# Kernel optimization log

Measured on AMD Instinct MI355X. Metric: run time of the kernel, lower is better.

## Reference

```python
import jax, jax.numpy as jnp
import numpy as np

N_NODES = 100000
N_EDGES = 600000
D = 128


def setup_inputs() -> dict:
    key = jax.random.key(0)
    k1, k2, k3, k4, k5, k6 = jax.random.split(key, 6)
    feat = jax.random.normal(k1, (N_NODES, D), dtype=jnp.float32)
    src = jax.random.randint(k2, (N_EDGES,), 0, N_NODES, dtype=jnp.int64)
    dst = jax.random.randint(k3, (N_EDGES,), 0, N_NODES, dtype=jnp.int64)
    W_neigh = jax.random.normal(k4, (D, D), dtype=jnp.float32) * (1.0 / np.sqrt(D))
    b_neigh = jax.random.normal(k5, (D,), dtype=jnp.float32) * 0.02
    W_self = jax.random.normal(k6, (D, D), dtype=jnp.float32) * (1.0 / np.sqrt(D))
    return {"feat": feat, "src": src, "dst": dst,
            "W_neigh": W_neigh, "b_neigh": b_neigh, "W_self": W_self}


def reference(feat, src, dst, W_neigh, b_neigh, W_self):
    # DGL GraphConv(norm='none'): sum-aggregate neighbor features, then linear.
    # agg[i] = sum_{(s->i) in E} feat[s]
    agg = jax.ops.segment_sum(feat[src], dst, num_segments=feat.shape[0])  # [N, D]
    neigh_feat = agg @ W_neigh + b_neigh                                   # [N, Dout]
    self_feat = feat @ W_self                                              # [N, Dout]
    return neigh_feat + self_feat
```

## Files before the change

### kernel.cpp

```cpp
#include <hip/hip_runtime.h>

#define DF 128
#define CAP 16
#define GR 64
#define PBLK 256

typedef __attribute__((ext_vector_type(8))) short short8;
typedef __attribute__((ext_vector_type(4))) float v4f;

__device__ __forceinline__ unsigned short f2bf(float x) {
    unsigned u = __float_as_uint(x);
    unsigned r = (u + 0x7FFFu + ((u >> 16) & 1u)) >> 16;
    return (unsigned short)r;
}
__device__ __forceinline__ float bf2f(unsigned short h) {
    return __uint_as_float((unsigned)h << 16);
}
__device__ __forceinline__ unsigned pack2(float a, float b) {
    return (unsigned)f2bf(a) | ((unsigned)f2bf(b) << 16);
}

__global__ __launch_bounds__(256) void prep_kernel(
    const int* __restrict__ idx32, int nE, int* __restrict__ hdr,
    const float* __restrict__ Wn, const float* __restrict__ Ws,
    unsigned short* __restrict__ Bt, int* __restrict__ counts, int cnt_ints,
    unsigned short* __restrict__ Ybf, int M)
{
    const int b = blockIdx.x;
    const int t = threadIdx.x;
    if (b == 0) {
        __shared__ int sh;
        if (t == 0) sh = 0;
        __syncthreads();
        int found = 0;
        for (int i = t; i < 2048 && i < nE; i += 256)
            if (idx32[2 * i + 1] != 0) found = 1;
        if (found) sh = 1;
        __syncthreads();
        if (t == 0) { hdr[0] = sh; hdr[1] = 0; }
        if (t < 64)
            reinterpret_cast<unsigned*>(Ybf + (size_t)M * DF)[t] = 0u;
    } else if (b <= 128) {
        int idx = (b - 1) * 256 + t;
        int n = idx >> 7, k = idx & 127;
        float v = (n < DF) ? Wn[(size_t)k * DF + n] : Ws[(size_t)k * DF + (n - DF)];
        Bt[idx] = f2bf(v);
    } else {
        int off = ((b - 129) * 256 + t) * 4;
        if (off < cnt_ints)
            *reinterpret_cast<int4*>(counts + off) = make_int4(0, 0, 0, 0);
    }
}

__global__ __launch_bounds__(256) void fused_kernel(
    const float* __restrict__ feat, const unsigned short* __restrict__ Bt,
    const float* __restrict__ bias, unsigned short* __restrict__ Ybf,
    float* __restrict__ out, int M,
    const void* __restrict__ src, const void* __restrict__ dst, int nE,
    int* __restrict__ hdr, int* __restrict__ counts, int* __restrict__ buckets,
    int2* __restrict__ ovf)
{
    const int t = threadIdx.x;

    if (blockIdx.x < PBLK) {
        const int is32 = hdr[0];
        const int stride = PBLK * 256;
        if (is32) {
            const int* sp = (const int*)src;
            const int* dp = (const int*)dst;
            for (int e = blockIdx.x * 256 + t; e < nE; e += stride) {
                int s = sp[e], d = dp[e];
                int pos = atomicAdd(&counts[d], 1);
                if (pos < CAP) {
                    buckets[(size_t)d * CAP + pos] = s;
                } else {
                    int oi = atomicAdd(&hdr[1], 1);
                    ovf[oi] = make_int2(s, d);
                }
            }
        } else {
            const long long* sp = (const long long*)src;
            const long long* dp = (const long long*)dst;
            for (int e = blockIdx.x * 256 + t; e < nE; e += stride) {
                int s = (int)sp[e], d = (int)dp[e];
                int pos = atomicAdd(&counts[d], 1);
                if (pos < CAP) {
                    buckets[(size_t)d * CAP + pos] = s;
                } else {
                    int oi = atomicAdd(&hdr[1], 1);
                    ovf[oi] = make_int2(s, d);
                }
            }
        }
        return;
    }

    __shared__ unsigned short As[GR][136];
    __shared__ unsigned short Ys[GR][136];

    const int wave = t >> 6;
    const int lane = t & 63;
    const int nl   = lane & 15;
    const int quad = lane >> 4;
    const int block_row = (blockIdx.x - PBLK) * GR;

    {
        const float* base = feat + (size_t)block_row * DF;
#pragma unroll
        for (int it = 0; it < 8; it++) {
            const int idx = t * 4 + it * 1024;
            const int row = idx >> 7, col = idx & 127;
            float4 v;
            if (block_row + row < M)
                v = *reinterpret_cast<const float4*>(base + idx);
            else
                v = make_float4(0.f, 0.f, 0.f, 0.f);
            uint2 pk;
            pk.x = pack2(v.x, v.y);
            pk.y = pack2(v.z, v.w);
            *reinterpret_cast<uint2*>(&As[row][col]) = pk;
        }
    }

    const int n0 = wave * 64;
    short8 bfrag[4][4];
#pragma unroll
    for (int ct = 0; ct < 4; ct++)
#pragma unroll
        for (int kk = 0; kk < 4; kk++)
            bfrag[ct][kk] = *reinterpret_cast<const short8*>(
                Bt + (size_t)(n0 + ct * 16 + nl) * DF + kk * 32 + quad * 8);

    float bcol[4];
#pragma unroll
    for (int ct = 0; ct < 4; ct++) {
        int n = n0 + ct * 16 + nl;
        bcol[ct] = (n >= DF) ? bias[n - DF] : 0.f;
    }

    __syncthreads();

#pragma unroll
    for (int rt = 0; rt < 4; rt++) {
        short8 afrag[4];
#pragma unroll
        for (int kk = 0; kk < 4; kk++)
            afrag[kk] = *reinterpret_cast<const short8*>(
                &As[rt * 16 + nl][kk * 32 + quad * 8]);
#pragma unroll
        for (int ct = 0; ct < 4; ct++) {
            v4f acc = {0.f, 0.f, 0.f, 0.f};
#pragma unroll
            for (int kk = 0; kk < 4; kk++)
                acc = __builtin_amdgcn_mfma_f32_16x16x32_bf16(
                    afrag[kk], bfrag[ct][kk], acc, 0, 0, 0);
            const int n = n0 + ct * 16 + nl;
            const int lrow = rt * 16 + quad * 4;
            if (n < DF) {
#pragma unroll
                for (int r = 0; r < 4; r++)
                    Ys[lrow + r][n] = f2bf(acc[r]);
            } else {
#pragma unroll
                for (int r = 0; r < 4; r++) {
                    const int grow = block_row + lrow + r;
                    if (grow < M)
                        out[(size_t)grow * DF + (n - DF)] = acc[r] + bcol[ct];
                }
            }
        }
    }

    __syncthreads();

    {
        const int row = t >> 2;
        const int cb  = (t & 3) * 32;
        const int grow = block_row + row;
        if (grow < M) {
            const uint4* srcp = reinterpret_cast<const uint4*>(&Ys[row][cb]);
            uint4* dstp = reinterpret_cast<uint4*>(Ybf + (size_t)grow * DF + cb);
            dstp[0] = srcp[0];
            dstp[1] = srcp[1];
            dstp[2] = srcp[2];
            dstp[3] = srcp[3];
        }
    }
}

__global__ __launch_bounds__(256) void gather_kernel(
    const unsigned short* __restrict__ Ybf,
    const int* __restrict__ counts, const int* __restrict__ buckets,
    const int* __restrict__ hdr, const int2* __restrict__ ovf,
    float* __restrict__ out, int M, int ngroups)
{
    const int gid  = blockIdx.x * 256 + threadIdx.x;
    const int grp  = gid >> 4;
    const int lane = gid & 15;
    const size_t lo = (size_t)lane * 8;

#define LDY(s) (*reinterpret_cast<const uint4*>(Ybf + (size_t)(s) * DF + lo))
#define ACC8(Y) do { \
        a0 += bf2f((unsigned short)((Y).x)); a1 += bf2f((unsigned short)((Y).x >> 16)); \
        a2 += bf2f((unsigned short)((Y).y)); a3 += bf2f((unsigned short)((Y).y >> 16)); \
        a4 += bf2f((unsigned short)((Y).z)); a5 += bf2f((unsigned short)((Y).z >> 16)); \
        a6 += bf2f((unsigned short)((Y).w)); a7 += bf2f((unsigned short)((Y).w >> 16)); \
    } while (0)

    if (grp < M) {
        const int node = grp;
        const int deg_raw = counts[node];
        const int deg = min(deg_raw, CAP);
        const int* b = buckets + (size_t)node * CAP;
        float* op = out + (size_t)node * DF + lo;

        float a0 = 0.f, a1 = 0.f, a2 = 0.f, a3 = 0.f;
        float a4 = 0.f, a5 = 0.f, a6 = 0.f, a7 = 0.f;

        int4 sa = *reinterpret_cast<const int4*>(b);
        int4 sb = *reinterpret_cast<const int4*>(b + 4);
        const int i0 = (0 < deg) ? sa.x : M;
        const int i1 = (1 < deg) ? sa.y : M;
        const int i2 = (2 < deg) ? sa.z : M;
        const int i3 = (3 < deg) ? sa.w : M;
        const int i4 = (4 < deg) ? sb.x : M;
        const int i5 = (5 < deg) ? sb.y : M;
        const int i6 = (6 < deg) ? sb.z : M;
        const int i7 = (7 < deg) ? sb.w : M;

        uint4 y0 = LDY(i0);
        uint4 y1 = LDY(i1);
        uint4 y2 = LDY(i2);
        uint4 y3 = LDY(i3);
        uint4 y4 = LDY(i4);
        uint4 y5 = LDY(i5);
        uint4 y6 = LDY(i6);
        uint4 y7 = LDY(i7);
        float4 o0 = *reinterpret_cast<const float4*>(op);
        float4 o1 = *reinterpret_cast<const float4*>(op + 4);
        __builtin_amdgcn_sched_barrier(0);
        ACC8(y0); ACC8(y1); ACC8(y2); ACC8(y3);
        ACC8(y4); ACC8(y5); ACC8(y6); ACC8(y7);

        if (deg > 8) {
            int4 sc = *reinterpret_cast<const int4*>(b + 8);
            int4 sd = *reinterpret_cast<const int4*>(b + 12);
            const int j0 = ( 8 < deg) ? sc.x : M;
            const int j1 = ( 9 < deg) ? sc.y : M;
            const int j2 = (10 < deg) ? sc.z : M;
            const int j3 = (11 < deg) ? sc.w : M;
            const int j4 = (12 < deg) ? sd.x : M;
            const int j5 = (13 < deg) ? sd.y : M;
            const int j6 = (14 < deg) ? sd.z : M;
            const int j7 = (15 < deg) ? sd.w : M;
            uint4 z0 = LDY(j0);
            uint4 z1 = LDY(j1);
            uint4 z2 = LDY(j2);
            uint4 z3 = LDY(j3);
            uint4 z4 = LDY(j4);
            uint4 z5 = LDY(j5);
            uint4 z6 = LDY(j6);
            uint4 z7 = LDY(j7);
            __builtin_amdgcn_sched_barrier(0);
            ACC8(z0); ACC8(z1); ACC8(z2); ACC8(z3);
            ACC8(z4); ACC8(z5); ACC8(z6); ACC8(z7);
        }

        if (deg_raw <= CAP) {
            o0.x += a0; o0.y += a1; o0.z += a2; o0.w += a3;
            o1.x += a4; o1.y += a5; o1.z += a6; o1.w += a7;
            *reinterpret_cast<float4*>(op)     = o0;
            *reinterpret_cast<float4*>(op + 4) = o1;
        } else {
            unsafeAtomicAdd(op + 0, a0);
            unsafeAtomicAdd(op + 1, a1);
            unsafeAtomicAdd(op + 2, a2);
            unsafeAtomicAdd(op + 3, a3);
            unsafeAtomicAdd(op + 4, a4);
            unsafeAtomicAdd(op + 5, a5);
            unsafeAtomicAdd(op + 6, a6);
            unsafeAtomicAdd(op + 7, a7);
        }
    }

    int n_ovf = hdr[1];
    for (int i = grp; i < n_ovf; i += ngroups) {
        int2 sd = ovf[i];
        uint4 y = LDY(sd.x);
        float* p = out + (size_t)sd.y * DF + lo;
        unsafeAtomicAdd(p + 0, bf2f((unsigned short)(y.x)));
        unsafeAtomicAdd(p + 1, bf2f((unsigned short)(y.x >> 16)));
        unsafeAtomicAdd(p + 2, bf2f((unsigned short)(y.y)));
        unsafeAtomicAdd(p + 3, bf2f((unsigned short)(y.y >> 16)));
        unsafeAtomicAdd(p + 4, bf2f((unsigned short)(y.z)));
        unsafeAtomicAdd(p + 5, bf2f((unsigned short)(y.z >> 16)));
        unsafeAtomicAdd(p + 6, bf2f((unsigned short)(y.w)));
        unsafeAtomicAdd(p + 7, bf2f((unsigned short)(y.w >> 16)));
    }
#undef LDY
#undef ACC8
}

extern "C" void kernel_launch(void* const* d_in, const int* in_sizes, int n_in,
                              void* d_out, int out_size, void* d_ws, size_t ws_size,
                              hipStream_t stream) {
    const float* feat = (const float*)d_in[0];
    const void*  src  = d_in[1];
    const void*  dst  = d_in[2];
    const float* Wn   = (const float*)d_in[3];
    const float* bias = (const float*)d_in[4];
    const float* Wsf  = (const float*)d_in[5];
    float* out = (float*)d_out;

    const int M  = in_sizes[0] / DF;
    const int nE = in_sizes[1];

    const size_t cnt_off   = 256;
    const size_t cnt_bytes = (((size_t)(M + 1) * 4) + 255) & ~(size_t)255;
    const size_t bkt_off   = cnt_off + cnt_bytes;
    const size_t bkt_bytes = (size_t)M * CAP * sizeof(int);
    const size_t bt_off    = (bkt_off + bkt_bytes + 255) & ~(size_t)255;
    const size_t bt_bytes  = (size_t)256 * DF * sizeof(unsigned short);
    const size_t y_off     = bt_off + bt_bytes;
    const size_t y_bytes   = (size_t)(M + 1) * DF * sizeof(unsigned short);
    const size_t ovf_off   = (y_off + y_bytes + 255) & ~(size_t)255;

    int*            hdr     = (int*)d_ws;
    int*            counts  = (int*)((char*)d_ws + cnt_off);
    int*            buckets = (int*)((char*)d_ws + bkt_off);
    unsigned short* Bt      = (unsigned short*)((char*)d_ws + bt_off);
    unsigned short* Ybf     = (unsigned short*)((char*)d_ws + y_off);
    int2*           ovf     = (int2*)((char*)d_ws + ovf_off);

    const int cnt_ints = (int)(cnt_bytes / 4);
    const int nzb = (cnt_ints + 1023) / 1024;
    prep_kernel<<<1 + 128 + nzb, 256, 0, stream>>>(
        (const int*)src, nE, hdr, Wn, Wsf, Bt, counts, cnt_ints, Ybf, M);

    const int gemm_blocks = (M + GR - 1) / GR;
    fused_kernel<<<PBLK + gemm_blocks, 256, 0, stream>>>(
        feat, Bt, bias, Ybf, out, M, src, dst, nE,
        hdr, counts, buckets, ovf);

    const int gablocks = (int)(((long long)M * 16 + 255) / 256);
    const int ngroups = gablocks * 16;
    gather_kernel<<<gablocks, 256, 0, stream>>>(
        Ybf, counts, buckets, hdr, ovf, out, M, ngroups);
}
```

Baseline: 193.9 us.

## Aggregate bf16 features before GEMM and fuse gather with combined K=256 matmul

Reorders the computation from transform-then-aggregate to aggregate-then-transform. Features are converted to bf16 in the prep kernel, and edge placement becomes its own kernel. A single kernel then gathers neighbour rows, builds a [agg | self] tile in shared memory, and runs one K=256 MFMA GEMM that writes the output once. This removes the Ybf intermediate write and read, plus the read-modify-write of out in the gather. The cost is a longer GEMM K dimension, an extra bf16 rounding of the aggregated sum, and a serial scan of the overflow list for high-degree nodes.

```diff
diff --git a/kernel.cpp b/kernel.cpp
--- a/kernel.cpp
+++ b/kernel.cpp
@@ -1,9 +1,10 @@
 #include <hip/hip_runtime.h>
 
 #define DF 128
+#define KX 256
 #define CAP 16
 #define GR 64
-#define PBLK 256
+#define PBLK 1024
 
 typedef __attribute__((ext_vector_type(8))) short short8;
 typedef __attribute__((ext_vector_type(4))) float v4f;
@@ -23,8 +24,9 @@
 __global__ __launch_bounds__(256) void prep_kernel(
     const int* __restrict__ idx32, int nE, int* __restrict__ hdr,
     const float* __restrict__ Wn, const float* __restrict__ Ws,
-    unsigned short* __restrict__ Bt, int* __restrict__ counts, int cnt_ints,
-    unsigned short* __restrict__ Ybf, int M)
+    unsigned short* __restrict__ Bt2, int* __restrict__ counts, int cnt_ints,
+    const float* __restrict__ feat, unsigned short* __restrict__ Fbf,
+    int M, int nzb)
 {
     const int b = blockIdx.x;
     const int t = threadIdx.x;
@@ -39,167 +41,106 @@
         __syncthreads();
         if (t == 0) { hdr[0] = sh; hdr[1] = 0; }
         if (t < 64)
-            reinterpret_cast<unsigned*>(Ybf + (size_t)M * DF)[t] = 0u;
+            reinterpret_cast<unsigned*>(Fbf + (size_t)M * DF)[t] = 0u;
     } else if (b <= 128) {
         int idx = (b - 1) * 256 + t;
-        int n = idx >> 7, k = idx & 127;
-        float v = (n < DF) ? Wn[(size_t)k * DF + n] : Ws[(size_t)k * DF + (n - DF)];
-        Bt[idx] = f2bf(v);
-    } else {
+        int n = idx >> 8, k = idx & 255;
+        float v = (k < DF) ? Wn[(size_t)k * DF + n]
+                           : Ws[(size_t)(k - DF) * DF + n];
+        Bt2[idx] = f2bf(v);
+    } else if (b <= 128 + nzb) {
         int off = ((b - 129) * 256 + t) * 4;
         if (off < cnt_ints)
             *reinterpret_cast<int4*>(counts + off) = make_int4(0, 0, 0, 0);
+    } else {
+        const long long base = ((long long)(b - 129 - nzb) * 2048 + t * 8);
+        const long long total = (long long)M * DF;
+        if (base + 8 <= total) {
+            float4 v0 = *reinterpret_cast<const float4*>(feat + base);
+            float4 v1 = *reinterpret_cast<const float4*>(feat + base + 4);
+            uint4 pk;
+            pk.x = pack2(v0.x, v0.y);
+            pk.y = pack2(v0.z, v0.w);
+            pk.z = pack2(v1.x, v1.y);
+            pk.w = pack2(v1.z, v1.w);
+            *reinterpret_cast<uint4*>(Fbf + base) = pk;
+        }
     }
 }
 
-__global__ __launch_bounds__(256) void fused_kernel(
-    const float* __restrict__ feat, const unsigned short* __restrict__ Bt,
-    const float* __restrict__ bias, unsigned short* __restrict__ Ybf,
-    float* __restrict__ out, int M,
+__global__ __launch_bounds__(256) void place_kernel(
     const void* __restrict__ src, const void* __restrict__ dst, int nE,
     int* __restrict__ hdr, int* __restrict__ counts, int* __restrict__ buckets,
     int2* __restrict__ ovf)
 {
     const int t = threadIdx.x;
-
-    if (blockIdx.x < PBLK) {
-        const int is32 = hdr[0];
-        const int stride = PBLK * 256;
-        if (is32) {
-            const int* sp = (const int*)src;
-            const int* dp = (const int*)dst;
-            for (int e = blockIdx.x * 256 + t; e < nE; e += stride) {
-                int s = sp[e], d = dp[e];
-                int pos = atomicAdd(&counts[d], 1);
-                if (pos < CAP) {
-                    buckets[(size_t)d * CAP + pos] = s;
-                } else {
-                    int oi = atomicAdd(&hdr[1], 1);
-                    ovf[oi] = make_int2(s, d);
-                }
-            }
-        } else {
-            const long long* sp = (const long long*)src;
-            const long long* dp = (const long long*)dst;
-            for (int e = blockIdx.x * 256 + t; e < nE; e += stride) {
-                int s = (int)sp[e], d = (int)dp[e];
-                int pos = atomicAdd(&counts[d], 1);
-                if (pos < CAP) {
-                    buckets[(size_t)d * CAP + pos] = s;
-                } else {
-                    int oi = atomicAdd(&hdr[1], 1);
-                    ovf[oi] = make_int2(s, d);
-                }
-            }
-        }
-        return;
+    const int is32 = hdr[0];
+    const int stride = PBLK * 256;
+    if (is32) {
+        const int* sp = (const int*)src;
+        const int* dp = (const int*)dst;
+        for (int e = blockIdx.x * 256 + t; e < nE; e += stride) {
+            int s = sp[e], d = dp[e];
+            int pos = atomicAdd(&counts[d], 1);
+            if (pos < CAP) {
+                buckets[(size_t)d * CAP + pos] = s;
+            } else {
+                int oi = atomicAdd(&hdr[1], 1);
+                ovf[oi] = make_int2(s, d);
+            }
+        }
+    } else {
+        const long long* sp = (const long long*)src;
+        const long long* dp = (const long long*)dst;
+        for (int e = blockIdx.x * 256 + t; e < nE; e += stride) {
+            int s = (int)sp[e], d = (int)dp[e];
+            int pos = atomicAdd(&counts[d], 1);
+            if (pos < CAP) {
+                buckets[(size_t)d * CAP + pos] = s;
+            } else {
+                int oi = atomicAdd(&hdr[1], 1);
+                ovf[oi] = make_int2(s, d);
+            }
+        }
     }
-
-    __shared__ unsigned short As[GR][136];
-    __shared__ unsigned short Ys[GR][136];
+}
+
+__global__ __launch_bounds__(256) void agg_gemm_kernel(
+    const unsigned short* __restrict__ Fbf, const unsigned short* __restrict__ Bt2,
+    const float* __restrict__ bias, float* __restrict__ out, int M,
+    const int* __restrict__ counts, const int* __restrict__ buckets,
+    const int* __restrict__ hdr, const int2* __restrict__ ovf)
+{
+    __shared__ unsigned short As[GR][KX + 8];
+
+    const int t = threadIdx.x;
+    const int block_row = blockIdx.x * GR;
 
     const int wave = t >> 6;
     const int lane = t & 63;
     const int nl   = lane & 15;
     const int quad = lane >> 4;
-    const int block_row = (blockIdx.x - PBLK) * GR;
+
+    const int n0 = wave * 32;
+    short8 bfrag[2][8];
+#pragma unroll
+    for (int ct = 0; ct < 2; ct++)
+#pragma unroll
+        for (int kk = 0; kk < 8; kk++)
+            bfrag[ct][kk] = *reinterpret_cast<const short8*>(
+                Bt2 + (size_t)(n0 + ct * 16 + nl) * KX + kk * 32 + quad * 8);
+    float bcol[2];
+#pragma unroll
+    for (int ct = 0; ct < 2; ct++)
+        bcol[ct] = bias[n0 + ct * 16 + nl];
 
     {
-        const float* base = feat + (size_t)block_row * DF;
-#pragma unroll
-        for (int it = 0; it < 8; it++) {
-            const int idx = t * 4 + it * 1024;
-            const int row = idx >> 7, col = idx & 127;
-            float4 v;
-            if (block_row + row < M)
-                v = *reinterpret_cast<const float4*>(base + idx);
-            else
-                v = make_float4(0.f, 0.f, 0.f, 0.f);
-            uint2 pk;
-            pk.x = pack2(v.x, v.y);
-            pk.y = pack2(v.z, v.w);
-            *reinterpret_cast<uint2*>(&As[row][col]) = pk;
-        }
-    }
-
-    const int n0 = wave * 64;
-    short8 bfrag[4][4];
-#pragma unroll
-    for (int ct = 0; ct < 4; ct++)
-#pragma unroll
-        for (int kk = 0; kk < 4; kk++)
-            bfrag[ct][kk] = *reinterpret_cast<const short8*>(
-                Bt + (size_t)(n0 + ct * 16 + nl) * DF + kk * 32 + quad * 8);
-
-    float bcol[4];
-#pragma unroll
-    for (int ct = 0; ct < 4; ct++) {
-        int n = n0 + ct * 16 + nl;
-        bcol[ct] = (n >= DF) ? bias[n - DF] : 0.f;
-    }
-
-    __syncthreads();
-
-#pragma unroll
-    for (int rt = 0; rt < 4; rt++) {
-        short8 afrag[4];
-#pragma unroll
-        for (int kk = 0; kk < 4; kk++)
-            afrag[kk] = *reinterpret_cast<const short8*>(
-                &As[rt * 16 + nl][kk * 32 + quad * 8]);
-#pragma unroll
-        for (int ct = 0; ct < 4; ct++) {
-            v4f acc = {0.f, 0.f, 0.f, 0.f};
-#pragma unroll
-            for (int kk = 0; kk < 4; kk++)
-                acc = __builtin_amdgcn_mfma_f32_16x16x32_bf16(
-                    afrag[kk], bfrag[ct][kk], acc, 0, 0, 0);
-            const int n = n0 + ct * 16 + nl;
-            const int lrow = rt * 16 + quad * 4;
-            if (n < DF) {
-#pragma unroll
-                for (int r = 0; r < 4; r++)
-                    Ys[lrow + r][n] = f2bf(acc[r]);
-            } else {
-#pragma unroll
-                for (int r = 0; r < 4; r++) {
-                    const int grow = block_row + lrow + r;
-                    if (grow < M)
-                        out[(size_t)grow * DF + (n - DF)] = acc[r] + bcol[ct];
-                }
-            }
-        }
-    }
-
-    __syncthreads();
-
-    {
-        const int row = t >> 2;
-        const int cb  = (t & 3) * 32;
-        const int grow = block_row + row;
-        if (grow < M) {
-            const uint4* srcp = reinterpret_cast<const uint4*>(&Ys[row][cb]);
-            uint4* dstp = reinterpret_cast<uint4*>(Ybf + (size_t)grow * DF + cb);
-            dstp[0] = srcp[0];
-            dstp[1] = srcp[1];
-            dstp[2] = srcp[2];
-            dstp[3] = srcp[3];
-        }
-    }
-}
-
-__global__ __launch_bounds__(256) void gather_kernel(
-    const unsigned short* __restrict__ Ybf,
-    const int* __restrict__ counts, const int* __restrict__ buckets,
-    const int* __restrict__ hdr, const int2* __restrict__ ovf,
-    float* __restrict__ out, int M, int ngroups)
-{
-    const int gid  = blockIdx.x * 256 + threadIdx.x;
-    const int grp  = gid >> 4;
-    const int lane = gid & 15;
-    const size_t lo = (size_t)lane * 8;
-
-#define LDY(s) (*reinterpret_cast<const uint4*>(Ybf + (size_t)(s) * DF + lo))
+        const int gi = t >> 4;
+        const int li = t & 15;
+        const size_t lo = (size_t)li * 8;
+        const int n_ovf = hdr[1];
+
+#define LDF(s) (*reinterpret_cast<const uint4*>(Fbf + (size_t)(s) * DF + lo))
 #define ACC8(Y) do { \
         a0 += bf2f((unsigned short)((Y).x)); a1 += bf2f((unsigned short)((Y).x >> 16)); \
         a2 += bf2f((unsigned short)((Y).y)); a3 += bf2f((unsigned short)((Y).y >> 16)); \
@@ -207,98 +148,110 @@
         a6 += bf2f((unsigned short)((Y).w)); a7 += bf2f((unsigned short)((Y).w >> 16)); \
     } while (0)
 
-    if (grp < M) {
-        const int node = grp;
-        const int deg_raw = counts[node];
-        const int deg = min(deg_raw, CAP);
-        const int* b = buckets + (size_t)node * CAP;
-        float* op = out + (size_t)node * DF + lo;
-
-        float a0 = 0.f, a1 = 0.f, a2 = 0.f, a3 = 0.f;
-        float a4 = 0.f, a5 = 0.f, a6 = 0.f, a7 = 0.f;
-
-        int4 sa = *reinterpret_cast<const int4*>(b);
-        int4 sb = *reinterpret_cast<const int4*>(b + 4);
-        const int i0 = (0 < deg) ? sa.x : M;
-        const int i1 = (1 < deg) ? sa.y : M;
-        const int i2 = (2 < deg) ? sa.z : M;
-        const int i3 = (3 < deg) ? sa.w : M;
-        const int i4 = (4 < deg) ? sb.x : M;
-        const int i5 = (5 < deg) ? sb.y : M;
-        const int i6 = (6 < deg) ? sb.z : M;
-        const int i7 = (7 < deg) ? sb.w : M;
-
-        uint4 y0 = LDY(i0);
-        uint4 y1 = LDY(i1);
-        uint4 y2 = LDY(i2);
-        uint4 y3 = LDY(i3);
-        uint4 y4 = LDY(i4);
-        uint4 y5 = LDY(i5);
-        uint4 y6 = LDY(i6);
-        uint4 y7 = LDY(i7);
-        float4 o0 = *reinterpret_cast<const float4*>(op);
-        float4 o1 = *reinterpret_cast<const float4*>(op + 4);
-        __builtin_amdgcn_sched_barrier(0);
-        ACC8(y0); ACC8(y1); ACC8(y2); ACC8(y3);
-        ACC8(y4); ACC8(y5); ACC8(y6); ACC8(y7);
-
-        if (deg > 8) {
-            int4 sc = *reinterpret_cast<const int4*>(b + 8);
-            int4 sd = *reinterpret_cast<const int4*>(b + 12);
-            const int j0 = ( 8 < deg) ? sc.x : M;
-            const int j1 = ( 9 < deg) ? sc.y : M;
-            const int j2 = (10 < deg) ? sc.z : M;
-            const int j3 = (11 < deg) ? sc.w : M;
-            const int j4 = (12 < deg) ? sd.x : M;
-            const int j5 = (13 < deg) ? sd.y : M;
-            const int j6 = (14 < deg) ? sd.z : M;
-            const int j7 = (15 < deg) ? sd.w : M;
-            uint4 z0 = LDY(j0);
-            uint4 z1 = LDY(j1);
-            uint4 z2 = LDY(j2);
-            uint4 z3 = LDY(j3);
-            uint4 z4 = LDY(j4);
-            uint4 z5 = LDY(j5);
-            uint4 z6 = LDY(j6);
-            uint4 z7 = LDY(j7);
-            __builtin_amdgcn_sched_barrier(0);
-            ACC8(z0); ACC8(z1); ACC8(z2); ACC8(z3);
-            ACC8(z4); ACC8(z5); ACC8(z6); ACC8(z7);
-        }
-
-        if (deg_raw <= CAP) {
-            o0.x += a0; o0.y += a1; o0.z += a2; o0.w += a3;
-            o1.x += a4; o1.y += a5; o1.z += a6; o1.w += a7;
-            *reinterpret_cast<float4*>(op)     = o0;
-            *reinterpret_cast<float4*>(op + 4) = o1;
-        } else {
-            unsafeAtomicAdd(op + 0, a0);
-            unsafeAtomicAdd(op + 1, a1);
-            unsafeAtomicAdd(op + 2, a2);
-            unsafeAtomicAdd(op + 3, a3);
-            unsafeAtomicAdd(op + 4, a4);
-            unsafeAtomicAdd(op + 5, a5);
-            unsafeAtomicAdd(op + 6, a6);
-            unsafeAtomicAdd(op + 7, a7);
-        }
+#pragma unroll
+        for (int j = 0; j < 4; j++) {
+            const int r_local = gi * 4 + j;
+            const int grow = block_row + r_local;
+            const int deg_raw = (grow < M) ? counts[grow] : 0;
+            const int deg = min(deg_raw, CAP);
+            const int* b = buckets + (size_t)((grow < M) ? grow : 0) * CAP;
+
+            float a0 = 0.f, a1 = 0.f, a2 = 0.f, a3 = 0.f;
+            float a4 = 0.f, a5 = 0.f, a6 = 0.f, a7 = 0.f;
+
+            int4 sa = *reinterpret_cast<const int4*>(b);
+            int4 sb = *reinterpret_cast<const int4*>(b + 4);
+            const int i0 = (0 < deg) ? sa.x : M;
+            const int i1 = (1 < deg) ? sa.y : M;
+            const int i2 = (2 < deg) ? sa.z : M;
+            const int i3 = (3 < deg) ? sa.w : M;
+            const int i4 = (4 < deg) ? sb.x : M;
+            const int i5 = (5 < deg) ? sb.y : M;
+            const int i6 = (6 < deg) ? sb.z : M;
+            const int i7 = (7 < deg) ? sb.w : M;
+            uint4 y0 = LDF(i0);
+            uint4 y1 = LDF(i1);
+            uint4 y2 = LDF(i2);
+            uint4 y3 = LDF(i3);
+            uint4 y4 = LDF(i4);
+            uint4 y5 = LDF(i5);
+            uint4 y6 = LDF(i6);
+            uint4 y7 = LDF(i7);
+            uint4 sf = LDF((grow < M) ? grow : M);
+            ACC8(y0); ACC8(y1); ACC8(y2); ACC8(y3);
+            ACC8(y4); ACC8(y5); ACC8(y6); ACC8(y7);
+
+            if (deg > 8) {
+                int4 sc = *reinterpret_cast<const int4*>(b + 8);
+                int4 sd = *reinterpret_cast<const int4*>(b + 12);
+                const int j0 = ( 8 < deg) ? sc.x : M;
+                const int j1 = ( 9 < deg) ? sc.y : M;
+                const int j2 = (10 < deg) ? sc.z : M;
+                const int j3 = (11 < deg) ? sc.w : M;
+                const int j4 = (12 < deg) ? sd.x : M;
+                const int j5 = (13 < deg) ? sd.y : M;
+                const int j6 = (14 < deg) ? sd.z : M;
+                const int j7 = (15 < deg) ? sd.w : M;
+                uint4 z0 = LDF(j0);
+                uint4 z1 = LDF(j1);
+                uint4 z2 = LDF(j2);
+                uint4 z3 = LDF(j3);
+                uint4 z4 = LDF(j4);
+                uint4 z5 = LDF(j5);
+                uint4 z6 = LDF(j6);
+                uint4 z7 = LDF(j7);
+                ACC8(z0); ACC8(z1); ACC8(z2); ACC8(z3);
+                ACC8(z4); ACC8(z5); ACC8(z6); ACC8(z7);
+            }
+
+            if (deg_raw > CAP) {
+                for (int i = 0; i < n_ovf; i++) {
+                    int2 sd2 = ovf[i];
+                    if (sd2.y == grow) {
+                        uint4 y = LDF(sd2.x);
+                        ACC8(y);
+                    }
+                }
+            }
+
+            uint4 pk;
+            pk.x = pack2(a0, a1);
+            pk.y = pack2(a2, a3);
+            pk.z = pack2(a4, a5);
+            pk.w = pack2(a6, a7);
+            *reinterpret_cast<uint4*>(&As[r_local][lo])      = pk;
+            *reinterpret_cast<uint4*>(&As[r_local][DF + lo]) = sf;
+        }
+#undef LDF
+#undef ACC8
     }
 
-    int n_ovf = hdr[1];
-    for (int i = grp; i < n_ovf; i += ngroups) {
-        int2 sd = ovf[i];
-        uint4 y = LDY(sd.x);
-        float* p = out + (size_t)sd.y * DF + lo;
-        unsafeAtomicAdd(p + 0, bf2f((unsigned short)(y.x)));
-        unsafeAtomicAdd(p + 1, bf2f((unsigned short)(y.x >> 16)));
-        unsafeAtomicAdd(p + 2, bf2f((unsigned short)(y.y)));
-        unsafeAtomicAdd(p + 3, bf2f((unsigned short)(y.y >> 16)));
-        unsafeAtomicAdd(p + 4, bf2f((unsigned short)(y.z)));
-        unsafeAtomicAdd(p + 5, bf2f((unsigned short)(y.z >> 16)));
-        unsafeAtomicAdd(p + 6, bf2f((unsigned short)(y.w)));
-        unsafeAtomicAdd(p + 7, bf2f((unsigned short)(y.w >> 16)));
+    __syncthreads();
+
+#pragma unroll
+    for (int rt = 0; rt < 4; rt++) {
+        short8 afrag[8];
+#pragma unroll
+        for (int kk = 0; kk < 8; kk++)
+            afrag[kk] = *reinterpret_cast<const short8*>(
+                &As[rt * 16 + nl][kk * 32 + quad * 8]);
+#pragma unroll
+        for (int ct = 0; ct < 2; ct++) {
+            v4f acc = {0.f, 0.f, 0.f, 0.f};
+#pragma unroll
+            for (int kk = 0; kk < 8; kk++)
+                acc = __builtin_amdgcn_mfma_f32_16x16x32_bf16(
+                    afrag[kk], bfrag[ct][kk], acc, 0, 0, 0);
+            const int n = n0 + ct * 16 + nl;
+            const int lrow = rt * 16 + quad * 4;
+#pragma unroll
+            for (int r = 0; r < 4; r++) {
+                const int grow = block_row + lrow + r;
+                if (grow < M)
+                    out[(size_t)grow * DF + n] = acc[r] + bcol[ct];
+            }
+        }
     }
-#undef LDY
-#undef ACC8
 }
 
 extern "C" void kernel_launch(void* const* d_in, const int* in_sizes, int n_in,
@@ -316,34 +269,35 @@
     const int nE = in_sizes[1];
 
     const size_t cnt_off   = 256;
-    const size_t cnt_bytes = (((size_t)(M + 1) * 4) + 255) & ~(size_t)255;
+    const size_t cnt_bytes = (((size_t)(M + 64) * 4) + 255) & ~(size_t)255;
     const size_t bkt_off   = cnt_off + cnt_bytes;
     const size_t bkt_bytes = (size_t)M * CAP * sizeof(int);
     const size_t bt_off    = (bkt_off + bkt_bytes + 255) & ~(size_t)255;
-    const size_t bt_bytes  = (size_t)256 * DF * sizeof(unsigned short);
-    const size_t y_off     = bt_off + bt_bytes;
-    const size_t y_bytes   = (size_t)(M + 1) * DF * sizeof(unsigned short);
-    const size_t ovf_off   = (y_off + y_bytes + 255) & ~(size_t)255;
+    const size_t bt_bytes  = (size_t)DF * KX * sizeof(unsigned short);
+    const size_t f_off     = bt_off + bt_bytes;
+    const size_t f_bytes   = (size_t)(M + 1) * DF * sizeof(unsigned short);
+    const size_t ovf_off   = (f_off + f_bytes + 255) & ~(size_t)255;
 
     int*            hdr     = (int*)d_ws;
     int*            counts  = (int*)((char*)d_ws + cnt_off);
     int*            buckets = (int*)((char*)d_ws + bkt_off);
-    unsigned short* Bt      = (unsigned short*)((char*)d_ws + bt_off);
-    unsigned short* Ybf     = (unsigned short*)((char*)d_ws + y_off);
+    unsigned short* Bt2     = (unsigned short*)((char*)d_ws + bt_off);
+    unsigned short* Fbf     = (unsigned short*)((char*)d_ws + f_off);
     int2*           ovf     = (int2*)((char*)d_ws + ovf_off);
 
     const int cnt_ints = (int)(cnt_bytes / 4);
     const int nzb = (cnt_ints + 1023) / 1024;
-    prep_kernel<<<1 + 128 + nzb, 256, 0, stream>>>(
-        (const int*)src, nE, hdr, Wn, Wsf, Bt, counts, cnt_ints, Ybf, M);
+    const long long total = (long long)M * DF;
+    const int nconv = (int)((total + 2047) / 2048);
+
+    prep_kernel<<<1 + 128 + nzb + nconv, 256, 0, stream>>>(
+        (const int*)src, nE, hdr, Wn, Wsf, Bt2, counts, cnt_ints,
+        feat, Fbf, M, nzb);
+
+    place_kernel<<<PBLK, 256, 0, stream>>>(
+        src, dst, nE, hdr, counts, buckets, ovf);
 
     const int gemm_blocks = (M + GR - 1) / GR;
-    fused_kernel<<<PBLK + gemm_blocks, 256, 0, stream>>>(
-        feat, Bt, bias, Ybf, out, M, src, dst, nE,
-        hdr, counts, buckets, ovf);
-
-    const int gablocks = (int)(((long long)M * 16 + 255) / 256);
-    const int ngroups = gablocks * 16;
-    gather_kernel<<<gablocks, 256, 0, stream>>>(
-        Ybf, counts, buckets, hdr, ovf, out, M, ngroups);
-}
+    agg_gemm_kernel<<<gemm_blocks, 256, 0, stream>>>(
+        Fbf, Bt2, bias, out, M, counts, buckets, hdr, ovf);
+}
```

After: 199.1 us. +2.7%, slower.
